# Kernel optimization log

Measured on AMD Instinct MI355X. Metric: run time of the kernel, lower is better.

Reference implementation:

```python
import jax, jax.numpy as jnp
import numpy as np

N_NODES = 50000
N_EDGES = 800000
IN_C, HID_C, OUT_C = 128, 128, 1


def setup_inputs() -> dict:
    key = jax.random.key(0)
    ks = jax.random.split(key, 10)
    x = jax.random.normal(ks[0], (N_NODES, IN_C), dtype=jnp.float32)
    x2 = jax.random.normal(ks[1], (1,), dtype=jnp.float32)
    edge_index = jax.random.randint(ks[2], (2, N_EDGES), 0, N_NODES, dtype=jnp.int64)
    # GCNConv params (glorot-ish scale) and final linear
    W1 = jax.random.normal(ks[3], (IN_C, HID_C), dtype=jnp.float32) / np.sqrt(IN_C)
    b1 = jnp.zeros((HID_C,), dtype=jnp.float32)
    W2 = jax.random.normal(ks[4], (HID_C, HID_C), dtype=jnp.float32) / np.sqrt(HID_C)
    b2 = jnp.zeros((HID_C,), dtype=jnp.float32)
    Wlin = jax.random.normal(ks[5], (HID_C, OUT_C), dtype=jnp.float32) / np.sqrt(HID_C)
    blin = jnp.zeros((OUT_C,), dtype=jnp.float32)
    return {"x": x, "x2": x2, "edge_index": edge_index, "num_nodes": N_NODES,
            "W1": W1, "b1": b1, "W2": W2, "b2": b2, "Wlin": Wlin, "blin": blin}


def _gcn_conv(h, W, b, src, dst, norm, num_nodes):
    # linear transform then normalized scatter-add aggregation (PyG GCNConv)
    h = h @ W  # [N, C_out]
    msg = h[src] * norm[:, None]  # gather + scale, [E+N, C_out]
    out = jax.ops.segment_sum(msg, dst, num_segments=num_nodes)
    return out + b


def _gcn_norm(edge_index, num_nodes):
    # add self-loops, compute sym-normalization coefficients D^-1/2 A D^-1/2
    loop = jnp.arange(num_nodes, dtype=edge_index.dtype)
    src = jnp.concatenate([edge_index[0], loop])
    dst = jnp.concatenate([edge_index[1], loop])
    ones = jnp.ones(src.shape[0], dtype=jnp.float32)
    deg = jax.ops.segment_sum(ones, dst, num_segments=num_nodes)
    dinv = jnp.where(deg > 0, jax.lax.rsqrt(deg), 0.0)
    norm = dinv[src] * dinv[dst]
    return src, dst, norm


def reference(x, x2, edge_index, num_nodes, W1, b1, W2, b2, Wlin, blin):
    src, dst, norm = _gcn_norm(edge_index, num_nodes)
    h = _gcn_conv(x, W1, b1, src, dst, norm, num_nodes)
    h = jax.nn.relu(h)
    # dropout is identity in eval mode
    h = _gcn_conv(h, W2, b2, src, dst, norm, num_nodes)
    h = jax.nn.relu(h)
    out = h @ Wlin + blin  # [N, 1]
    return out.squeeze(-1)
```

## Files before the change

### kernel.cpp

```cpp
#include <hip/hip_runtime.h>
#include <hip/hip_bf16.h>

#define N_NODES 50000
#define N_EDGES 800000
#define C 128

#define NBB   391
#define CAPB  3072
#define CAPC  3456
#define CHUNK 2048

typedef __attribute__((ext_vector_type(8))) short short8v;
typedef __attribute__((ext_vector_type(4))) float f32x4;

__device__ __forceinline__ unsigned int bf16rtn(float f) {
    unsigned int u = __float_as_uint(f);
    return (u + 0x7fffu + ((u >> 16) & 1u)) >> 16;
}
__device__ __forceinline__ unsigned int packbf2(float lo, float hi) {
    return bf16rtn(lo) | (bf16rtn(hi) << 16);
}

__global__ void k_prepW(const float* __restrict__ W1, const float* __restrict__ W2,
                        unsigned short* __restrict__ Wsplit, int* __restrict__ gcur) {
    int t = blockIdx.x * 256 + threadIdx.x;
    if (t < NBB) gcur[t] = 0;
    if (t >= 32768) return;
    int layer = t >> 14, idx = t & 16383;
    int i = idx >> 7, j = idx & 127;
    const float* Wsrc = layer ? W2 : W1;
    float w = Wsrc[i * 128 + j];
    unsigned int h = bf16rtn(w);
    float hf = __uint_as_float(h << 16);
    unsigned int l = bf16rtn(w - hf);
    unsigned short* base = Wsplit + layer * 32768;
    base[j * 128 + i] = (unsigned short)h;
    base[16384 + j * 128 + i] = (unsigned short)l;
}

__global__ __launch_bounds__(256) void k_binA(const int* __restrict__ ei,
                                              int* __restrict__ gcur,
                                              int2* __restrict__ tmp) {
    __shared__ int hist[NBB];
    __shared__ int lbase[NBB];
    __shared__ int gbaseL[NBB];
    __shared__ int wsum[4];
    __shared__ int2 buf[CHUNK];
    __shared__ int totalv;

    int tid = threadIdx.x;
    int e0 = blockIdx.x * CHUNK;

    for (int i = tid; i < NBB; i += 256) hist[i] = 0;
    __syncthreads();

    int sarr[8], darr[8], parr[8];
#pragma unroll
    for (int j = 0; j < 8; ++j) {
        int e = e0 + j * 256 + tid;
        darr[j] = -1;
        if (e < N_EDGES) {
            sarr[j] = ei[e];
            int d = ei[N_EDGES + e];
            darr[j] = d;
            parr[j] = atomicAdd(&hist[d >> 7], 1);
        }
    }
    __syncthreads();

    {
        int i0 = 2 * tid, i1 = i0 + 1;
        int c0 = (i0 < NBB) ? hist[i0] : 0;
        int c1 = (i1 < NBB) ? hist[i1] : 0;
        int c = c0 + c1;
        int lane = tid & 63, w = tid >> 6;
        int s = c;
#pragma unroll
        for (int d = 1; d < 64; d <<= 1) {
            int u = __shfl_up(s, d, 64);
            if (lane >= d) s += u;
        }
        if (lane == 63) wsum[w] = s;
        __syncthreads();
        int add = 0;
        for (int i = 0; i < w; ++i) add += wsum[i];
        int incl = s + add;
        int excl = incl - c;
        if (i0 < NBB) lbase[i0] = excl;
        if (i1 < NBB) lbase[i1] = excl + c0;
        if (tid == 255) totalv = incl;
    }
    for (int i = tid; i < NBB; i += 256) {
        int cnt = hist[i];
        int run = (cnt > 0) ? atomicAdd(&gcur[i], cnt) : 0;
        gbaseL[i] = i * CAPB + run;
    }
    __syncthreads();

#pragma unroll
    for (int j = 0; j < 8; ++j) {
        if (darr[j] >= 0) {
            int b = darr[j] >> 7;
            buf[lbase[b] + parr[j]] = make_int2(sarr[j], darr[j]);
        }
    }
    __syncthreads();

    int total = totalv;
    for (int i = tid; i < total; i += 256) {
        int2 v = buf[i];
        int b = v.y >> 7;
        int gpos = gbaseL[b] + (i - lbase[b]);
        if (gpos < (b + 1) * CAPB) tmp[gpos] = v;
    }
}

__global__ __launch_bounds__(256) void k_csr(const int2* __restrict__ tmp,
                                             const int* __restrict__ gcur,
                                             int* __restrict__ csr,
                                             int* __restrict__ offn,
                                             int* __restrict__ degn,
                                             float* __restrict__ dinv) {
    __shared__ int   rawsrc[CAPB];
    __shared__ short rawloc[CAPB];
    __shared__ int   lcnt[128];
    __shared__ int   lbase[128];
    __shared__ int   lcur[128];

    int b = blockIdx.x, tid = threadIdx.x;
    int cnt = gcur[b];
    if (cnt > CAPB) cnt = CAPB;

    if (tid < 128) { lcnt[tid] = 0; lcur[tid] = 0; }
    __syncthreads();

    const int2* tmpb = tmp + (size_t)b * CAPB;
    for (int i = tid; i < cnt; i += 256) {
        int2 v = tmpb[i];
        int l = v.y & 127;
        rawsrc[i] = v.x;
        rawloc[i] = (short)l;
        atomicAdd(&lcnt[l], 1);
    }
    __syncthreads();

    if (tid < 64) {
        int c0 = lcnt[2 * tid], c1 = lcnt[2 * tid + 1];
        int p0 = (c0 + 3) & ~3, p1 = (c1 + 3) & ~3;
        int c = p0 + p1;
        int s = c;
#pragma unroll
        for (int d = 1; d < 64; d <<= 1) {
            int u = __shfl_up(s, d, 64);
            if (tid >= d) s += u;
        }
        int excl = s - c;
        lbase[2 * tid] = excl;
        lbase[2 * tid + 1] = excl + p0;
    }
    __syncthreads();

    int node = b * 128 + tid;
    if (tid < 128 && node < N_NODES) {
        offn[node] = b * CAPC + lbase[tid];
        degn[node] = lcnt[tid];
        dinv[node] = rsqrtf((float)lcnt[tid] + 1.0f);
    }

    for (int i = tid; i < cnt; i += 256) {
        int l = rawloc[i];
        int p = atomicAdd(&lcur[l], 1);
        csr[b * CAPC + lbase[l] + p] = rawsrc[i];
    }
}

template <bool AF32>
__global__ __launch_bounds__(512, 4) void k_gemm(const void* __restrict__ Ain,
                                                 const unsigned short* __restrict__ Whg,
                                                 const unsigned short* __restrict__ Wlg,
                                                 const float* __restrict__ dinv,
                                                 unsigned short* __restrict__ Hout) {
    __shared__ uint4 Al[64 * 16];
    __shared__ float ddv[64];

    int tid = threadIdx.x;
    int row0 = blockIdx.x * 64;
    int wv = tid >> 6, lane = tid & 63;
    int col = wv * 16 + (lane & 15);
    int kq = lane >> 4;

    const uint4* Bh4 = (const uint4*)Whg;
    const uint4* Bl4 = (const uint4*)Wlg;
    short8v bh[4], bl[4];
#pragma unroll
    for (int ks = 0; ks < 4; ++ks) {
        uint4 uh = Bh4[col * 16 + ks * 4 + kq];
        uint4 ul = Bl4[col * 16 + ks * 4 + kq];
        bh[ks] = *reinterpret_cast<short8v*>(&uh);
        bl[ks] = *reinterpret_cast<short8v*>(&ul);
    }

#pragma unroll
    for (int pass = 0; pass < 2; ++pass) {
        int row = (tid >> 4) + pass * 32;
        int o = tid & 15;
        int gr = row0 + row;
        uint4 u = make_uint4(0u, 0u, 0u, 0u);
        if (AF32) {
            float4 v0 = make_float4(0.f, 0.f, 0.f, 0.f), v1 = v0;
            if (gr < N_NODES) {
                const float4* A4 = (const float4*)Ain;
                v0 = A4[gr * 32 + o * 2];
                v1 = A4[gr * 32 + o * 2 + 1];
            }
            u.x = packbf2(v0.x, v0.y);
            u.y = packbf2(v0.z, v0.w);
            u.z = packbf2(v1.x, v1.y);
            u.w = packbf2(v1.z, v1.w);
        } else {
            if (gr < N_NODES) u = ((const uint4*)Ain)[gr * 16 + o];
        }
        int byte = (row * 256 + o * 16) ^ ((row & 7) << 4);
        Al[byte >> 4] = u;
    }
    if (tid < 64) {
        int gr = row0 + tid;
        ddv[tid] = (gr < N_NODES) ? dinv[gr] : 0.f;
    }
    __syncthreads();

    f32x4 acc[4];
#pragma unroll
    for (int st = 0; st < 4; ++st) acc[st] = (f32x4){0.f, 0.f, 0.f, 0.f};

#pragma unroll
    for (int st = 0; st < 4; ++st) {
        int rowl = st * 16 + (lane & 15);
        int rbase = rowl * 256;
        int swz = (rowl & 7) << 4;
#pragma unroll
        for (int ks = 0; ks < 4; ++ks) {
            int byte = (rbase + ks * 64 + kq * 16) ^ swz;
            uint4 ua = Al[byte >> 4];
            short8v a = *reinterpret_cast<short8v*>(&ua);
            acc[st] = __builtin_amdgcn_mfma_f32_16x16x32_bf16(a, bh[ks], acc[st], 0, 0, 0);
            acc[st] = __builtin_amdgcn_mfma_f32_16x16x32_bf16(a, bl[ks], acc[st], 0, 0, 0);
        }
    }

#pragma unroll
    for (int st = 0; st < 4; ++st) {
#pragma unroll
        for (int r = 0; r < 4; ++r) {
            int rowl = st * 16 + kq * 4 + r;
            int gr = row0 + rowl;
            if (gr < N_NODES) {
                float dv = ddv[rowl];
                Hout[gr * 128 + col] = (unsigned short)bf16rtn(dv * acc[st][r]);
            }
        }
    }
}

__device__ __forceinline__ void add8(float* acc, uint4 u) {
    acc[0] += __uint_as_float(u.x << 16);
    acc[1] += __uint_as_float(u.x & 0xffff0000u);
    acc[2] += __uint_as_float(u.y << 16);
    acc[3] += __uint_as_float(u.y & 0xffff0000u);
    acc[4] += __uint_as_float(u.z << 16);
    acc[5] += __uint_as_float(u.z & 0xffff0000u);
    acc[6] += __uint_as_float(u.w << 16);
    acc[7] += __uint_as_float(u.w & 0xffff0000u);
}

template <bool FINAL>
__global__ __launch_bounds__(256) void k_agg(const uint4* __restrict__ h4,
                                             const int* __restrict__ csr,
                                             const int* __restrict__ offn,
                                             const int* __restrict__ degn,
                                             const float* __restrict__ bias,
                                             const float* __restrict__ Wlin,
                                             const float* __restrict__ blin,
                                             void* __restrict__ aggout) {
    int n = (blockIdx.x * 256 + threadIdx.x) >> 6;
    int lane = threadIdx.x & 63, eg = lane >> 4, cq = lane & 15;

    int o0 = offn[n];
    int deg = degn[n];
    int end = o0 + deg;

    uint4 us = h4[n * 16 + cq];

    float acc[8];
#pragma unroll
    for (int j = 0; j < 8; ++j) acc[j] = 0.f;

    int e = o0;
    for (; e + 16 <= end; e += 16) {
        int4 s4 = *(const int4*)(csr + e + 4 * eg);
        uint4 u0 = h4[s4.x * 16 + cq];
        uint4 u1 = h4[s4.y * 16 + cq];
        uint4 u2 = h4[s4.z * 16 + cq];
        uint4 u3 = h4[s4.w * 16 + cq];
        add8(acc, u0); add8(acc, u1); add8(acc, u2); add8(acc, u3);
    }
    if (e + 8 <= end) {
        int2 s2 = *(const int2*)(csr + e + 2 * eg);
        uint4 u0 = h4[s2.x * 16 + cq];
        uint4 u1 = h4[s2.y * 16 + cq];
        add8(acc, u0); add8(acc, u1);
        e += 8;
    }
    {
        int r = end - e;
        int b0 = e + 2 * eg;
        if (2 * eg < r)     add8(acc, h4[csr[b0] * 16 + cq]);
        if (2 * eg + 1 < r) add8(acc, h4[csr[b0 + 1] * 16 + cq]);
    }
#pragma unroll
    for (int j = 0; j < 8; ++j) {
        acc[j] += __shfl_xor(acc[j], 16, 64);
        acc[j] += __shfl_xor(acc[j], 32, 64);
    }

    float dv = rsqrtf((float)deg + 1.0f);
    float4 bv0 = ((const float4*)bias)[cq * 2];
    float4 bv1 = ((const float4*)bias)[cq * 2 + 1];
    float hv[8];
    hv[0] = __uint_as_float(us.x << 16); hv[1] = __uint_as_float(us.x & 0xffff0000u);
    hv[2] = __uint_as_float(us.y << 16); hv[3] = __uint_as_float(us.y & 0xffff0000u);
    hv[4] = __uint_as_float(us.z << 16); hv[5] = __uint_as_float(us.z & 0xffff0000u);
    hv[6] = __uint_as_float(us.w << 16); hv[7] = __uint_as_float(us.w & 0xffff0000u);
    float o[8];
    o[0] = dv * (acc[0] + hv[0]) + bv0.x;
    o[1] = dv * (acc[1] + hv[1]) + bv0.y;
    o[2] = dv * (acc[2] + hv[2]) + bv0.z;
    o[3] = dv * (acc[3] + hv[3]) + bv0.w;
    o[4] = dv * (acc[4] + hv[4]) + bv1.x;
    o[5] = dv * (acc[5] + hv[5]) + bv1.y;
    o[6] = dv * (acc[6] + hv[6]) + bv1.z;
    o[7] = dv * (acc[7] + hv[7]) + bv1.w;

    if (!FINAL) {
        if (eg == 0) {
            uint4 u;
            u.x = packbf2(fmaxf(o[0], 0.f), fmaxf(o[1], 0.f));
            u.y = packbf2(fmaxf(o[2], 0.f), fmaxf(o[3], 0.f));
            u.z = packbf2(fmaxf(o[4], 0.f), fmaxf(o[5], 0.f));
            u.w = packbf2(fmaxf(o[6], 0.f), fmaxf(o[7], 0.f));
            ((uint4*)aggout)[n * 16 + cq] = u;
        }
    } else {
        float4 wl0 = ((const float4*)Wlin)[cq * 2];
        float4 wl1 = ((const float4*)Wlin)[cq * 2 + 1];
        float v = fmaxf(o[0], 0.f) * wl0.x + fmaxf(o[1], 0.f) * wl0.y
                + fmaxf(o[2], 0.f) * wl0.z + fmaxf(o[3], 0.f) * wl0.w
                + fmaxf(o[4], 0.f) * wl1.x + fmaxf(o[5], 0.f) * wl1.y
                + fmaxf(o[6], 0.f) * wl1.z + fmaxf(o[7], 0.f) * wl1.w;
        v += __shfl_xor(v, 1, 64);
        v += __shfl_xor(v, 2, 64);
        v += __shfl_xor(v, 4, 64);
        v += __shfl_xor(v, 8, 64);
        if (lane == 0) ((float*)aggout)[n] = v + blin[0];
    }
}

extern "C" void kernel_launch(void* const* d_in, const int* in_sizes, int n_in,
                              void* d_out, int out_size, void* d_ws, size_t ws_size,
                              hipStream_t stream) {
    const float* x    = (const float*)d_in[0];
    const int*   ei   = (const int*)d_in[2];
    const float* W1   = (const float*)d_in[4];
    const float* b1   = (const float*)d_in[5];
    const float* W2   = (const float*)d_in[6];
    const float* b2   = (const float*)d_in[7];
    const float* Wlin = (const float*)d_in[8];
    const float* blin = (const float*)d_in[9];
    float* out = (float*)d_out;

    char* ws = (char*)d_ws;
    size_t off = 0;
    auto carve = [&](size_t bytes) -> void* {
        void* p = ws + off;
        off = (off + bytes + 255) & ~(size_t)255;
        return p;
    };
    int*   gcur = (int*)  carve(NBB * sizeof(int));
    float* dinv = (float*)carve(N_NODES * sizeof(float));
    int*   offn = (int*)  carve(N_NODES * sizeof(int));
    int*   degn = (int*)  carve(N_NODES * sizeof(int));
    int2*  tmp  = (int2*) carve((size_t)NBB * CAPB * sizeof(int2));
    int*   csr  = (int*)  carve((size_t)NBB * CAPC * sizeof(int));
    unsigned short* hbf  = (unsigned short*)carve((size_t)N_NODES * C * sizeof(unsigned short));
    unsigned short* hbf2 = (unsigned short*)carve((size_t)N_NODES * C * sizeof(unsigned short));
    unsigned short* wsplit = (unsigned short*)carve(4 * 16384 * sizeof(unsigned short));

    const int NB_A = (N_EDGES + CHUNK - 1) / CHUNK;
    const int NB_G = (N_NODES + 63) / 64;
    const int NB_W = (N_NODES * 64) / 256;

    const unsigned short* W1h = wsplit;
    const unsigned short* W1l = wsplit + 16384;
    const unsigned short* W2h = wsplit + 32768;
    const unsigned short* W2l = wsplit + 49152;

    k_prepW<<<128, 256, 0, stream>>>(W1, W2, wsplit, gcur);
    k_binA<<<NB_A, 256, 0, stream>>>(ei, gcur, tmp);
    k_csr<<<NBB, 256, 0, stream>>>(tmp, gcur, csr, offn, degn, dinv);

    k_gemm<true><<<NB_G, 512, 0, stream>>>(x, W1h, W1l, dinv, hbf);
    k_agg<false><<<NB_W, 256, 0, stream>>>((const uint4*)hbf, csr, offn, degn,
                                           b1, Wlin, blin, hbf2);
    k_gemm<false><<<NB_G, 512, 0, stream>>>(hbf2, W2h, W2l, dinv, hbf);
    k_agg<true><<<NB_W, 256, 0, stream>>>((const uint4*)hbf, csr, offn, degn,
                                          b2, Wlin, blin, out);
}
```

Baseline: 202.8 us.

## Split hidden features into four column slices for cache-local aggregation

Stores the bf16 hidden features as four 32-column slices, each a contiguous 3.2 MB array, so every aggregation block gathers from one slice small enough to stay cache-resident. Blocks are ordered slice-major, and each node's edges are spread over four sub-lanes with a shuffle reduction. The final layer now writes per-slice partial dot products that a new small kernel sums. The cost is re-reading the CSR indices once per slice, narrower 64-byte gathers, and an extra launch and partial buffer.

```diff
diff --git a/kernel.cpp b/kernel.cpp
--- a/kernel.cpp
+++ b/kernel.cpp
@@ -9,6 +9,11 @@
 #define CAPB  3072
 #define CAPC  3456
 #define CHUNK 2048
+
+#define NSL     4
+#define SL_U4   200000
+#define SL_US   1600000
+#define BPS     3125
 
 typedef __attribute__((ext_vector_type(8))) short short8v;
 typedef __attribute__((ext_vector_type(4))) float f32x4;
@@ -218,7 +223,8 @@
             u.z = packbf2(v1.x, v1.y);
             u.w = packbf2(v1.z, v1.w);
         } else {
-            if (gr < N_NODES) u = ((const uint4*)Ain)[gr * 16 + o];
+            if (gr < N_NODES)
+                u = ((const uint4*)Ain)[(size_t)(o >> 2) * SL_U4 + gr * 4 + (o & 3)];
         }
         int byte = (row * 256 + o * 16) ^ ((row & 7) << 4);
         Al[byte >> 4] = u;
@@ -248,15 +254,17 @@
         }
     }
 
-#pragma unroll
-    for (int st = 0; st < 4; ++st) {
-#pragma unroll
-        for (int r = 0; r < 4; ++r) {
-            int rowl = st * 16 + kq * 4 + r;
-            int gr = row0 + rowl;
-            if (gr < N_NODES) {
-                float dv = ddv[rowl];
-                Hout[gr * 128 + col] = (unsigned short)bf16rtn(dv * acc[st][r]);
+    {
+        int sl = col >> 5, cs = col & 31;
+        unsigned short* Hs = Hout + (size_t)sl * SL_US + cs;
+#pragma unroll
+        for (int st = 0; st < 4; ++st) {
+#pragma unroll
+            for (int r = 0; r < 4; ++r) {
+                int rowl = st * 16 + kq * 4 + r;
+                int gr = row0 + rowl;
+                if (gr < N_NODES)
+                    Hs[gr * 32] = (unsigned short)bf16rtn(ddv[rowl] * acc[st][r]);
             }
         }
     }
@@ -274,63 +282,53 @@
 }
 
 template <bool FINAL>
-__global__ __launch_bounds__(256) void k_agg(const uint4* __restrict__ h4,
+__global__ __launch_bounds__(256) void k_agg(const uint4* __restrict__ hall,
                                              const int* __restrict__ csr,
                                              const int* __restrict__ offn,
                                              const int* __restrict__ degn,
                                              const float* __restrict__ bias,
                                              const float* __restrict__ Wlin,
-                                             const float* __restrict__ blin,
-                                             void* __restrict__ aggout) {
-    int n = (blockIdx.x * 256 + threadIdx.x) >> 6;
-    int lane = threadIdx.x & 63, eg = lane >> 4, cq = lane & 15;
+                                             void* __restrict__ outbuf) {
+    int bid = blockIdx.x;
+    int slice = bid / BPS;
+    int nb = bid - slice * BPS;
+    int wv = threadIdx.x >> 6, lane = threadIdx.x & 63;
+    int j = lane >> 4;
+    int sub = (lane >> 2) & 3;
+    int cq = lane & 3;
+    int n = nb * 16 + wv * 4 + j;
+
+    const uint4* hs = hall + (size_t)slice * SL_U4;
 
     int o0 = offn[n];
     int deg = degn[n];
+    uint4 us = hs[n * 4 + cq];
+
+    float acc[8];
+#pragma unroll
+    for (int k = 0; k < 8; ++k) acc[k] = 0.f;
+
+    int e = o0 + sub;
     int end = o0 + deg;
-
-    uint4 us = h4[n * 16 + cq];
-
-    float acc[8];
-#pragma unroll
-    for (int j = 0; j < 8; ++j) acc[j] = 0.f;
-
-    int e = o0;
-    for (; e + 16 <= end; e += 16) {
-        int4 s4 = *(const int4*)(csr + e + 4 * eg);
-        uint4 u0 = h4[s4.x * 16 + cq];
-        uint4 u1 = h4[s4.y * 16 + cq];
-        uint4 u2 = h4[s4.z * 16 + cq];
-        uint4 u3 = h4[s4.w * 16 + cq];
-        add8(acc, u0); add8(acc, u1); add8(acc, u2); add8(acc, u3);
-    }
-    if (e + 8 <= end) {
-        int2 s2 = *(const int2*)(csr + e + 2 * eg);
-        uint4 u0 = h4[s2.x * 16 + cq];
-        uint4 u1 = h4[s2.y * 16 + cq];
-        add8(acc, u0); add8(acc, u1);
-        e += 8;
-    }
-    {
-        int r = end - e;
-        int b0 = e + 2 * eg;
-        if (2 * eg < r)     add8(acc, h4[csr[b0] * 16 + cq]);
-        if (2 * eg + 1 < r) add8(acc, h4[csr[b0 + 1] * 16 + cq]);
-    }
-#pragma unroll
-    for (int j = 0; j < 8; ++j) {
-        acc[j] += __shfl_xor(acc[j], 16, 64);
-        acc[j] += __shfl_xor(acc[j], 32, 64);
+    for (; e < end; e += 4) {
+        int s = __builtin_nontemporal_load(csr + e);
+        uint4 u = hs[s * 4 + cq];
+        add8(acc, u);
+    }
+#pragma unroll
+    for (int k = 0; k < 8; ++k) {
+        acc[k] += __shfl_xor(acc[k], 4, 64);
+        acc[k] += __shfl_xor(acc[k], 8, 64);
     }
 
     float dv = rsqrtf((float)deg + 1.0f);
-    float4 bv0 = ((const float4*)bias)[cq * 2];
-    float4 bv1 = ((const float4*)bias)[cq * 2 + 1];
     float hv[8];
     hv[0] = __uint_as_float(us.x << 16); hv[1] = __uint_as_float(us.x & 0xffff0000u);
     hv[2] = __uint_as_float(us.y << 16); hv[3] = __uint_as_float(us.y & 0xffff0000u);
     hv[4] = __uint_as_float(us.z << 16); hv[5] = __uint_as_float(us.z & 0xffff0000u);
     hv[6] = __uint_as_float(us.w << 16); hv[7] = __uint_as_float(us.w & 0xffff0000u);
+    float4 bv0 = ((const float4*)bias)[slice * 8 + cq * 2];
+    float4 bv1 = ((const float4*)bias)[slice * 8 + cq * 2 + 1];
     float o[8];
     o[0] = dv * (acc[0] + hv[0]) + bv0.x;
     o[1] = dv * (acc[1] + hv[1]) + bv0.y;
@@ -342,27 +340,34 @@
     o[7] = dv * (acc[7] + hv[7]) + bv1.w;
 
     if (!FINAL) {
-        if (eg == 0) {
+        if (sub == 0) {
             uint4 u;
             u.x = packbf2(fmaxf(o[0], 0.f), fmaxf(o[1], 0.f));
             u.y = packbf2(fmaxf(o[2], 0.f), fmaxf(o[3], 0.f));
             u.z = packbf2(fmaxf(o[4], 0.f), fmaxf(o[5], 0.f));
             u.w = packbf2(fmaxf(o[6], 0.f), fmaxf(o[7], 0.f));
-            ((uint4*)aggout)[n * 16 + cq] = u;
+            ((uint4*)outbuf)[(size_t)slice * SL_U4 + n * 4 + cq] = u;
         }
     } else {
-        float4 wl0 = ((const float4*)Wlin)[cq * 2];
-        float4 wl1 = ((const float4*)Wlin)[cq * 2 + 1];
+        float4 wl0 = ((const float4*)Wlin)[slice * 8 + cq * 2];
+        float4 wl1 = ((const float4*)Wlin)[slice * 8 + cq * 2 + 1];
         float v = fmaxf(o[0], 0.f) * wl0.x + fmaxf(o[1], 0.f) * wl0.y
                 + fmaxf(o[2], 0.f) * wl0.z + fmaxf(o[3], 0.f) * wl0.w
                 + fmaxf(o[4], 0.f) * wl1.x + fmaxf(o[5], 0.f) * wl1.y
                 + fmaxf(o[6], 0.f) * wl1.z + fmaxf(o[7], 0.f) * wl1.w;
         v += __shfl_xor(v, 1, 64);
         v += __shfl_xor(v, 2, 64);
-        v += __shfl_xor(v, 4, 64);
-        v += __shfl_xor(v, 8, 64);
-        if (lane == 0) ((float*)aggout)[n] = v + blin[0];
-    }
+        if ((lane & 15) == 0)
+            __builtin_nontemporal_store(v, (float*)outbuf + slice * N_NODES + n);
+    }
+}
+
+__global__ void k_fin(const float* __restrict__ partial, const float* __restrict__ blin,
+                      float* __restrict__ out) {
+    int n = blockIdx.x * 256 + threadIdx.x;
+    if (n < N_NODES)
+        out[n] = ((partial[n] + partial[N_NODES + n])
+                + (partial[2 * N_NODES + n] + partial[3 * N_NODES + n])) + blin[0];
 }
 
 extern "C" void kernel_launch(void* const* d_in, const int* in_sizes, int n_in,
@@ -391,13 +396,15 @@
     int*   degn = (int*)  carve(N_NODES * sizeof(int));
     int2*  tmp  = (int2*) carve((size_t)NBB * CAPB * sizeof(int2));
     int*   csr  = (int*)  carve((size_t)NBB * CAPC * sizeof(int));
-    unsigned short* hbf  = (unsigned short*)carve((size_t)N_NODES * C * sizeof(unsigned short));
-    unsigned short* hbf2 = (unsigned short*)carve((size_t)N_NODES * C * sizeof(unsigned short));
+    unsigned short* hbf  = (unsigned short*)carve((size_t)NSL * SL_US * sizeof(unsigned short));
+    unsigned short* hbf2 = (unsigned short*)carve((size_t)NSL * SL_US * sizeof(unsigned short));
+    float* partial = (float*)carve((size_t)NSL * N_NODES * sizeof(float));
     unsigned short* wsplit = (unsigned short*)carve(4 * 16384 * sizeof(unsigned short));
 
     const int NB_A = (N_EDGES + CHUNK - 1) / CHUNK;
     const int NB_G = (N_NODES + 63) / 64;
-    const int NB_W = (N_NODES * 64) / 256;
+    const int NB_S = NSL * BPS;
+    const int NB_F = (N_NODES + 255) / 256;
 
     const unsigned short* W1h = wsplit;
     const unsigned short* W1l = wsplit + 16384;
@@ -409,9 +416,10 @@
     k_csr<<<NBB, 256, 0, stream>>>(tmp, gcur, csr, offn, degn, dinv);
 
     k_gemm<true><<<NB_G, 512, 0, stream>>>(x, W1h, W1l, dinv, hbf);
-    k_agg<false><<<NB_W, 256, 0, stream>>>((const uint4*)hbf, csr, offn, degn,
-                                           b1, Wlin, blin, hbf2);
+    k_agg<false><<<NB_S, 256, 0, stream>>>((const uint4*)hbf, csr, offn, degn,
+                                           b1, Wlin, hbf2);
     k_gemm<false><<<NB_G, 512, 0, stream>>>(hbf2, W2h, W2l, dinv, hbf);
-    k_agg<true><<<NB_W, 256, 0, stream>>>((const uint4*)hbf, csr, offn, degn,
-                                          b2, Wlin, blin, out);
-}
+    k_agg<true><<<NB_S, 256, 0, stream>>>((const uint4*)hbf, csr, offn, degn,
+                                          b2, Wlin, partial);
+    k_fin<<<NB_F, 256, 0, stream>>>(partial, blin, out);
+}
```

Result: slower. 238.1 us (+17.4%).

## Pack edge binning records into 32 bits and store CSR sources as uint16

Applied to the files above, without the earlier changes.

The binning pass now packs each edge's source id and local destination slot into one 32-bit word instead of an int2. The CSR source array is stored as 16-bit indices, which works because node ids stay below 65536. This halves the bytes moved through the temporary bin buffer and the CSR index reads in both aggregation passes, and reduces shared-memory use in the CSR build. CAPC is raised so per-bin CSR segments stay aligned for the narrower vector loads; the change hard-wires the assumption that node ids fit in 16 bits.

```diff
diff --git a/kernel.cpp b/kernel.cpp
--- a/kernel.cpp
+++ b/kernel.cpp
@@ -7,7 +7,7 @@
 
 #define NBB   391
 #define CAPB  3072
-#define CAPC  3456
+#define CAPC  3584
 #define CHUNK 2048
 
 typedef __attribute__((ext_vector_type(8))) short short8v;
@@ -40,12 +40,13 @@
 
 __global__ __launch_bounds__(256) void k_binA(const int* __restrict__ ei,
                                               int* __restrict__ gcur,
-                                              int2* __restrict__ tmp) {
+                                              unsigned int* __restrict__ tmp) {
     __shared__ int hist[NBB];
     __shared__ int lbase[NBB];
     __shared__ int gbaseL[NBB];
     __shared__ int wsum[4];
-    __shared__ int2 buf[CHUNK];
+    __shared__ unsigned int  bufp[CHUNK];
+    __shared__ unsigned short bufb[CHUNK];
     __shared__ int totalv;
 
     int tid = threadIdx.x;
@@ -54,16 +55,18 @@
     for (int i = tid; i < NBB; i += 256) hist[i] = 0;
     __syncthreads();
 
-    int sarr[8], darr[8], parr[8];
+    unsigned int pkarr[8];
+    int barr[8], parr[8];
 #pragma unroll
     for (int j = 0; j < 8; ++j) {
         int e = e0 + j * 256 + tid;
-        darr[j] = -1;
+        barr[j] = -1;
         if (e < N_EDGES) {
-            sarr[j] = ei[e];
+            int s = ei[e];
             int d = ei[N_EDGES + e];
-            darr[j] = d;
-            parr[j] = atomicAdd(&hist[d >> 7], 1);
+            pkarr[j] = (unsigned int)s | ((unsigned int)(d & 127) << 20);
+            barr[j] = d >> 7;
+            parr[j] = atomicAdd(&hist[barr[j]], 1);
         }
     }
     __syncthreads();
@@ -99,33 +102,32 @@
 
 #pragma unroll
     for (int j = 0; j < 8; ++j) {
-        if (darr[j] >= 0) {
-            int b = darr[j] >> 7;
-            buf[lbase[b] + parr[j]] = make_int2(sarr[j], darr[j]);
+        if (barr[j] >= 0) {
+            int pos = lbase[barr[j]] + parr[j];
+            bufp[pos] = pkarr[j];
+            bufb[pos] = (unsigned short)barr[j];
         }
     }
     __syncthreads();
 
     int total = totalv;
     for (int i = tid; i < total; i += 256) {
-        int2 v = buf[i];
-        int b = v.y >> 7;
+        int b = bufb[i];
         int gpos = gbaseL[b] + (i - lbase[b]);
-        if (gpos < (b + 1) * CAPB) tmp[gpos] = v;
-    }
-}
-
-__global__ __launch_bounds__(256) void k_csr(const int2* __restrict__ tmp,
+        if (gpos < (b + 1) * CAPB) tmp[gpos] = bufp[i];
+    }
+}
+
+__global__ __launch_bounds__(256) void k_csr(const unsigned int* __restrict__ tmp,
                                              const int* __restrict__ gcur,
-                                             int* __restrict__ csr,
+                                             unsigned short* __restrict__ csr,
                                              int* __restrict__ offn,
                                              int* __restrict__ degn,
                                              float* __restrict__ dinv) {
-    __shared__ int   rawsrc[CAPB];
-    __shared__ short rawloc[CAPB];
-    __shared__ int   lcnt[128];
-    __shared__ int   lbase[128];
-    __shared__ int   lcur[128];
+    __shared__ unsigned int raw[CAPB];
+    __shared__ int lcnt[128];
+    __shared__ int lbase[128];
+    __shared__ int lcur[128];
 
     int b = blockIdx.x, tid = threadIdx.x;
     int cnt = gcur[b];
@@ -134,13 +136,11 @@
     if (tid < 128) { lcnt[tid] = 0; lcur[tid] = 0; }
     __syncthreads();
 
-    const int2* tmpb = tmp + (size_t)b * CAPB;
+    const unsigned int* tmpb = tmp + (size_t)b * CAPB;
     for (int i = tid; i < cnt; i += 256) {
-        int2 v = tmpb[i];
-        int l = v.y & 127;
-        rawsrc[i] = v.x;
-        rawloc[i] = (short)l;
-        atomicAdd(&lcnt[l], 1);
+        unsigned int v = tmpb[i];
+        raw[i] = v;
+        atomicAdd(&lcnt[v >> 20], 1);
     }
     __syncthreads();
 
@@ -168,9 +168,10 @@
     }
 
     for (int i = tid; i < cnt; i += 256) {
-        int l = rawloc[i];
+        unsigned int v = raw[i];
+        int l = v >> 20;
         int p = atomicAdd(&lcur[l], 1);
-        csr[b * CAPC + lbase[l] + p] = rawsrc[i];
+        csr[b * CAPC + lbase[l] + p] = (unsigned short)(v & 0xFFFFFu);
     }
 }
 
@@ -275,7 +276,7 @@
 
 template <bool FINAL>
 __global__ __launch_bounds__(256) void k_agg(const uint4* __restrict__ h4,
-                                             const int* __restrict__ csr,
+                                             const unsigned short* __restrict__ csr,
                                              const int* __restrict__ offn,
                                              const int* __restrict__ degn,
                                              const float* __restrict__ bias,
@@ -297,25 +298,25 @@
 
     int e = o0;
     for (; e + 16 <= end; e += 16) {
-        int4 s4 = *(const int4*)(csr + e + 4 * eg);
-        uint4 u0 = h4[s4.x * 16 + cq];
-        uint4 u1 = h4[s4.y * 16 + cq];
-        uint4 u2 = h4[s4.z * 16 + cq];
-        uint4 u3 = h4[s4.w * 16 + cq];
+        ushort4 s4 = *(const ushort4*)(csr + e + 4 * eg);
+        uint4 u0 = h4[(int)s4.x * 16 + cq];
+        uint4 u1 = h4[(int)s4.y * 16 + cq];
+        uint4 u2 = h4[(int)s4.z * 16 + cq];
+        uint4 u3 = h4[(int)s4.w * 16 + cq];
         add8(acc, u0); add8(acc, u1); add8(acc, u2); add8(acc, u3);
     }
     if (e + 8 <= end) {
-        int2 s2 = *(const int2*)(csr + e + 2 * eg);
-        uint4 u0 = h4[s2.x * 16 + cq];
-        uint4 u1 = h4[s2.y * 16 + cq];
+        ushort2 s2 = *(const ushort2*)(csr + e + 2 * eg);
+        uint4 u0 = h4[(int)s2.x * 16 + cq];
+        uint4 u1 = h4[(int)s2.y * 16 + cq];
         add8(acc, u0); add8(acc, u1);
         e += 8;
     }
     {
         int r = end - e;
         int b0 = e + 2 * eg;
-        if (2 * eg < r)     add8(acc, h4[csr[b0] * 16 + cq]);
-        if (2 * eg + 1 < r) add8(acc, h4[csr[b0 + 1] * 16 + cq]);
+        if (2 * eg < r)     add8(acc, h4[(int)csr[b0] * 16 + cq]);
+        if (2 * eg + 1 < r) add8(acc, h4[(int)csr[b0 + 1] * 16 + cq]);
     }
 #pragma unroll
     for (int j = 0; j < 8; ++j) {
@@ -389,8 +390,8 @@
     float* dinv = (float*)carve(N_NODES * sizeof(float));
     int*   offn = (int*)  carve(N_NODES * sizeof(int));
     int*   degn = (int*)  carve(N_NODES * sizeof(int));
-    int2*  tmp  = (int2*) carve((size_t)NBB * CAPB * sizeof(int2));
-    int*   csr  = (int*)  carve((size_t)NBB * CAPC * sizeof(int));
+    unsigned int*   tmp = (unsigned int*)  carve((size_t)NBB * CAPB * sizeof(unsigned int));
+    unsigned short* csr = (unsigned short*)carve((size_t)NBB * CAPC * sizeof(unsigned short));
     unsigned short* hbf  = (unsigned short*)carve((size_t)N_NODES * C * sizeof(unsigned short));
     unsigned short* hbf2 = (unsigned short*)carve((size_t)N_NODES * C * sizeof(unsigned short));
     unsigned short* wsplit = (unsigned short*)carve(4 * 16384 * sizeof(unsigned short));
```

New measurement: 200.3 us. About the same (-1.2%).
